# Kernel optimization log

Hardware: AMD Instinct MI355X
Metric: run time of the kernel (lower is better)

Reference implementation:

```python
import jax, jax.numpy as jnp
import numpy as np

B, S = 4, 2048
IN_F, OUT_F = 4096, 4096
BLK = 8
NB_IN = IN_F // BLK   # 512
NB_OUT = OUT_F // BLK  # 512


def setup_inputs() -> dict:
    key = jax.random.key(0)
    k_x, k_c = jax.random.split(key)
    x = jax.random.normal(k_x, (B, S, IN_F), dtype=jnp.float32)
    # mimic xavier_uniform on (NB_OUT*NB_IN, BLK) then / sqrt(BLK)
    bound = float(np.sqrt(6.0 / (NB_OUT * NB_IN + BLK)))
    circ_params = jax.random.uniform(k_c, (NB_OUT, NB_IN, BLK), dtype=jnp.float32,
                                     minval=-bound, maxval=bound) / np.sqrt(BLK)
    bias = jnp.zeros((OUT_F,), dtype=jnp.float32)
    return {"x": x, "circ_params": circ_params, "bias": bias}


def reference(x, circ_params, bias):
    # x: (B, S, IN_F) -> (B, S, NB_IN, BLK)
    xb = x.reshape(*x.shape[:-1], NB_IN, BLK)
    x_rfft = jnp.fft.rfft(xb, axis=-1)              # (B, S, NB_IN, BLK//2+1) complex
    c_rfft = jnp.fft.rfft(circ_params, axis=-1)     # (NB_OUT, NB_IN, BLK//2+1) complex
    # per-frequency block contraction: sum over input blocks i
    out_rfft = jnp.einsum('bsif,nif->bsnf', x_rfft, c_rfft)  # (B, S, NB_OUT, BLK//2+1)
    out = jnp.fft.irfft(out_rfft, n=BLK, axis=-1)   # (B, S, NB_OUT, BLK)
    out = out.reshape(*x.shape[:-1], OUT_F)
    return out + bias
```

## Files before the change

kernel.cpp:

```cpp
#include <hip/hip_runtime.h>

#define AS1 __attribute__((address_space(1)))
#define AS3 __attribute__((address_space(3)))

typedef __attribute__((ext_vector_type(8))) short short8;
typedef __attribute__((ext_vector_type(4))) float floatx4;
typedef __attribute__((ext_vector_type(8))) unsigned short u16x8;
typedef __attribute__((ext_vector_type(4))) unsigned short u16x4;
typedef __attribute__((ext_vector_type(4))) float f32x4;

#define M_DIM 8192
#define K_DIM 4096
#define N_DIM 4096
#define NB    512

#define SQ2H 0.70710678118654752f

#define P0_OFF 0
#define P1_OFF 4194304
#define P2_OFF 12582912
#define P3_OFF 20971520
#define P4_OFF 29360128
#define Q0_OFF 0
#define Q1_OFF 262144
#define Q2_OFF 1310720
#define Q3_OFF 2359296
#define Q4_OFF 3407872

static __device__ __forceinline__ unsigned short f32_to_bf16(float f) {
  union { float f; unsigned int u; } v;
  v.f = f;
  return (unsigned short)((v.u + 0x7FFFu + ((v.u >> 16) & 1u)) >> 16);
}
static __device__ __forceinline__ float bf16_to_f32(unsigned short h) {
  union { unsigned int u; float f; } v;
  v.u = ((unsigned int)h) << 16;
  return v.f;
}

struct F8 { float a0, a4, r1, i1, r2, i2, r3, i3; };
static __device__ __forceinline__ F8 rfft8(const float* x) {
  F8 o;
  o.a0 = x[0]+x[1]+x[2]+x[3]+x[4]+x[5]+x[6]+x[7];
  o.a4 = x[0]-x[1]+x[2]-x[3]+x[4]-x[5]+x[6]-x[7];
  const float d1 = x[1]-x[3]-x[5]+x[7];
  const float s1 = x[1]+x[3]-x[5]-x[7];
  o.r1 = x[0]-x[4] + SQ2H*d1;
  o.i1 = -(SQ2H*s1 + x[2]-x[6]);
  o.r2 = x[0]-x[2]+x[4]-x[6];
  o.i2 = -(x[1]-x[3]+x[5]-x[7]);
  o.r3 = x[0]-x[4] - SQ2H*d1;
  o.i3 = -(SQ2H*s1 - x[2]+x[6]);
  return o;
}


__global__ __launch_bounds__(256) void xtransform_kernel(
    const float* __restrict__ x, unsigned short* __restrict__ XF)
{
  const int tid = blockIdx.x * 256 + threadIdx.x;
  const int m  = tid >> 7;
  const int i4 = tid & 127;
  float v[32];
#pragma unroll
  for (int q = 0; q < 8; ++q)
    *reinterpret_cast<f32x4*>(v + q * 4) =
        *reinterpret_cast<const f32x4*>(x + (size_t)m * 4096 + i4 * 32 + q * 4);

  u16x4 p0, p4;
  u16x8 p1, p2, p3;
#pragma unroll
  for (int g = 0; g < 4; ++g) {
    F8 f = rfft8(v + g * 8);
    p0[g] = f32_to_bf16(f.a0);
    p4[g] = f32_to_bf16(f.a4);
    p1[2*g] = f32_to_bf16(f.r1); p1[2*g+1] = f32_to_bf16(f.i1);
    p2[2*g] = f32_to_bf16(f.r2); p2[2*g+1] = f32_to_bf16(f.i2);
    p3[2*g] = f32_to_bf16(f.r3); p3[2*g+1] = f32_to_bf16(f.i3);
  }
  *reinterpret_cast<u16x4*>(XF + P0_OFF + (size_t)m * 512 + i4 * 4) = p0;
  *reinterpret_cast<u16x4*>(XF + P4_OFF + (size_t)m * 512 + i4 * 4) = p4;
  *reinterpret_cast<u16x8*>(XF + P1_OFF + (size_t)m * 1024 + i4 * 8) = p1;
  *reinterpret_cast<u16x8*>(XF + P2_OFF + (size_t)m * 1024 + i4 * 8) = p2;
  *reinterpret_cast<u16x8*>(XF + P3_OFF + (size_t)m * 1024 + i4 * 8) = p3;
}

__global__ __launch_bounds__(256) void wtransform_kernel(
    const float* __restrict__ c, unsigned short* __restrict__ WF)
{
  const int tid = blockIdx.x * 256 + threadIdx.x;
  const int n = tid >> 9;
  const int i = tid & 511;
  float v[8];
  *reinterpret_cast<f32x4*>(v)     = *reinterpret_cast<const f32x4*>(c + (size_t)tid * 8);
  *reinterpret_cast<f32x4*>(v + 4) = *reinterpret_cast<const f32x4*>(c + (size_t)tid * 8 + 4);
  F8 f = rfft8(v);
  WF[Q0_OFF + (size_t)n * 512 + i] = f32_to_bf16(f.a0);
  WF[Q4_OFF + (size_t)n * 512 + i] = f32_to_bf16(f.a4);
  unsigned int q1or = (unsigned int)f32_to_bf16(f.r1) | ((unsigned int)f32_to_bf16(-f.i1) << 16);
  unsigned int q1oi = (unsigned int)f32_to_bf16(f.i1) | ((unsigned int)f32_to_bf16(f.r1) << 16);
  unsigned int q2or = (unsigned int)f32_to_bf16(f.r2) | ((unsigned int)f32_to_bf16(-f.i2) << 16);
  unsigned int q2oi = (unsigned int)f32_to_bf16(f.i2) | ((unsigned int)f32_to_bf16(f.r2) << 16);
  unsigned int q3or = (unsigned int)f32_to_bf16(f.r3) | ((unsigned int)f32_to_bf16(-f.i3) << 16);
  unsigned int q3oi = (unsigned int)f32_to_bf16(f.i3) | ((unsigned int)f32_to_bf16(f.r3) << 16);
  *reinterpret_cast<unsigned int*>(WF + Q1_OFF + (size_t)n * 1024 + 2 * i)         = q1or;
  *reinterpret_cast<unsigned int*>(WF + Q1_OFF + (size_t)(512 + n) * 1024 + 2 * i) = q1oi;
  *reinterpret_cast<unsigned int*>(WF + Q2_OFF + (size_t)n * 1024 + 2 * i)         = q2or;
  *reinterpret_cast<unsigned int*>(WF + Q2_OFF + (size_t)(512 + n) * 1024 + 2 * i) = q2oi;
  *reinterpret_cast<unsigned int*>(WF + Q3_OFF + (size_t)n * 1024 + 2 * i)         = q3or;
  *reinterpret_cast<unsigned int*>(WF + Q3_OFF + (size_t)(512 + n) * 1024 + 2 * i) = q3oi;
}

__global__ __launch_bounds__(256) void gemm_freq_kernel(
    const unsigned short* __restrict__ XF,
    const unsigned short* __restrict__ WF,
    unsigned short* __restrict__ OF)
{
  const int bid = blockIdx.x;
  const int swz = (bid & 7) * 256 + (bid >> 3);
  const int mt  = swz >> 5;
  const int yf  = swz & 31;
  int z, nt;
  if (yf < 4)       { z = 0; nt = yf; }
  else if (yf < 28) { z = 1 + ((yf - 4) >> 3); nt = (yf - 4) & 7; }
  else              { z = 4; nt = yf - 28; }

  int K, aoff, boff;
  switch (z) {
    case 0:  K = 512;  aoff = P0_OFF; boff = Q0_OFF; break;
    case 1:  K = 1024; aoff = P1_OFF; boff = Q1_OFF; break;
    case 2:  K = 1024; aoff = P2_OFF; boff = Q2_OFF; break;
    case 3:  K = 1024; aoff = P3_OFF; boff = Q3_OFF; break;
    default: K = 512;  aoff = P4_OFF; boff = Q4_OFF; break;
  }
  const int n0 = nt * 128;
  const int m0 = mt * 128;

  const unsigned short* A  = XF + aoff;
  const unsigned short* Bm = WF + boff;
  unsigned short* C        = OF + aoff;

  __shared__ alignas(16) unsigned short As[128 * 32];
  __shared__ alignas(16) unsigned short Bs[128 * 32];

  const int tid  = threadIdx.x;
  const int lane = tid & 63;
  const int wave = tid >> 6;
  const int wm   = wave >> 1;
  const int wn   = wave & 1;
  const int quad = lane >> 4;
  const int l15  = lane & 15;

  floatx4 acc[4][4];
#pragma unroll
  for (int i = 0; i < 4; ++i)
#pragma unroll
    for (int j = 0; j < 4; ++j) acc[i][j] = (floatx4){0.f, 0.f, 0.f, 0.f};

  for (int k0 = 0; k0 < K; k0 += 32) {
#pragma unroll
    for (int j = 0; j < 2; ++j) {
      const int chunk = j * 256 + wave * 64 + lane;
      const int row   = chunk >> 2;
      const int kc    = (chunk & 3) << 3;
      const unsigned short* ga = A  + (size_t)(m0 + row) * K + (k0 + kc);
      const unsigned short* gb = Bm + (size_t)(n0 + row) * K + (k0 + kc);
      unsigned short* la = As + (j * 256 + wave * 64) * 8;
      unsigned short* lb = Bs + (j * 256 + wave * 64) * 8;
      __builtin_amdgcn_global_load_lds((AS1 void*)ga, (AS3 void*)la, 16, 0, 0);
      __builtin_amdgcn_global_load_lds((AS1 void*)gb, (AS3 void*)lb, 16, 0, 0);
    }
    __syncthreads();

    short8 af[4], bf[4];
#pragma unroll
    for (int mi = 0; mi < 4; ++mi)
      af[mi] = *reinterpret_cast<const short8*>(As + (wm * 64 + mi * 16 + l15) * 32 + quad * 8);
#pragma unroll
    for (int ni = 0; ni < 4; ++ni)
      bf[ni] = *reinterpret_cast<const short8*>(Bs + (wn * 64 + ni * 16 + l15) * 32 + quad * 8);

#pragma unroll
    for (int mi = 0; mi < 4; ++mi)
#pragma unroll
      for (int ni = 0; ni < 4; ++ni)
        acc[mi][ni] = __builtin_amdgcn_mfma_f32_16x16x32_bf16(
            af[mi], bf[ni], acc[mi][ni], 0, 0, 0);
    __syncthreads();
  }

#pragma unroll
  for (int mi = 0; mi < 4; ++mi) {
#pragma unroll
    for (int r = 0; r < 4; ++r) {
      const int grow = m0 + wm * 64 + mi * 16 + quad * 4 + r;
      unsigned short* crow = C + (size_t)grow * K;
#pragma unroll
      for (int ni = 0; ni < 4; ++ni)
        crow[n0 + wn * 64 + ni * 16 + l15] = f32_to_bf16(acc[mi][ni][r]);
    }
  }
}

__global__ __launch_bounds__(256) void irfft_kernel(
    const unsigned short* __restrict__ OF,
    const float* __restrict__ bias,
    float* __restrict__ out)
{
  __shared__ alignas(16) float lds[256 * 36];
  const int t   = threadIdx.x;
  const int gt  = blockIdx.x * 256 + t;
  const int m   = gt >> 7;
  const int nb4 = gt & 127;

  const u16x4 a0v = *reinterpret_cast<const u16x4*>(OF + P0_OFF + (size_t)m * 512 + nb4 * 4);
  const u16x4 a4v = *reinterpret_cast<const u16x4*>(OF + P4_OFF + (size_t)m * 512 + nb4 * 4);
  const u16x4 r1v = *reinterpret_cast<const u16x4*>(OF + P1_OFF + (size_t)m * 1024 + nb4 * 4);
  const u16x4 i1v = *reinterpret_cast<const u16x4*>(OF + P1_OFF + (size_t)m * 1024 + 512 + nb4 * 4);
  const u16x4 r2v = *reinterpret_cast<const u16x4*>(OF + P2_OFF + (size_t)m * 1024 + nb4 * 4);
  const u16x4 i2v = *reinterpret_cast<const u16x4*>(OF + P2_OFF + (size_t)m * 1024 + 512 + nb4 * 4);
  const u16x4 r3v = *reinterpret_cast<const u16x4*>(OF + P3_OFF + (size_t)m * 1024 + nb4 * 4);
  const u16x4 i3v = *reinterpret_cast<const u16x4*>(OF + P3_OFF + (size_t)m * 1024 + 512 + nb4 * 4);

  float res[32];
#pragma unroll
  for (int j = 0; j < 4; ++j) {
    const int nblk = nb4 * 4 + j;
    const float a0 = bf16_to_f32(a0v[j]), a4 = bf16_to_f32(a4v[j]);
    const float r1 = bf16_to_f32(r1v[j]), i1 = bf16_to_f32(i1v[j]);
    const float r2 = bf16_to_f32(r2v[j]), i2 = bf16_to_f32(i2v[j]);
    const float r3 = bf16_to_f32(r3v[j]), i3 = bf16_to_f32(i3v[j]);

    const float ep = a0 + a4, em = a0 - a4;
    const float sr1 = SQ2H * r1, si1 = SQ2H * i1;
    const float sr3 = SQ2H * r3, si3 = SQ2H * i3;
    float o[8];
    o[0] = (ep + 2.f * ( r1 + r2 + r3)) * 0.125f;
    o[1] = (em + 2.f * ( sr1 - si1 - i2 - sr3 - si3)) * 0.125f;
    o[2] = (ep + 2.f * (-i1 - r2 + i3)) * 0.125f;
    o[3] = (em + 2.f * (-sr1 - si1 + i2 + sr3 - si3)) * 0.125f;
    o[4] = (ep + 2.f * (-r1 + r2 - r3)) * 0.125f;
    o[5] = (em + 2.f * (-sr1 + si1 - i2 + sr3 + si3)) * 0.125f;
    o[6] = (ep + 2.f * ( i1 - r2 - i3)) * 0.125f;
    o[7] = (em + 2.f * ( sr1 + si1 + i2 - sr3 + si3)) * 0.125f;

    const f32x4 blo = *reinterpret_cast<const f32x4*>(bias + nblk * 8);
    const f32x4 bhi = *reinterpret_cast<const f32x4*>(bias + nblk * 8 + 4);
#pragma unroll
    for (int k = 0; k < 4; ++k) {
      res[j * 8 + k]     = o[k]     + blo[k];
      res[j * 8 + 4 + k] = o[k + 4] + bhi[k];
    }
  }

  float* dst = lds + t * 36;
#pragma unroll
  for (int p = 0; p < 8; ++p)
    *reinterpret_cast<f32x4*>(dst + p * 4) = *reinterpret_cast<const f32x4*>(res + p * 4);
  __syncthreads();

  float* gbase = out + (size_t)blockIdx.x * 8192;
#pragma unroll
  for (int s = 0; s < 8; ++s) {
    const int off16 = s * 256 + t;
    const f32x4 vv = *reinterpret_cast<const f32x4*>(
        lds + (off16 >> 3) * 36 + (off16 & 7) * 4);
    *reinterpret_cast<f32x4*>(gbase + off16 * 4) = vv;
  }
}


__global__ __launch_bounds__(256) void convert_x_kernel(
    const float* __restrict__ x, unsigned short* __restrict__ Xb)
{
  const size_t t = (size_t)blockIdx.x * 256 + threadIdx.x;
  const f32x4 a = *reinterpret_cast<const f32x4*>(x + t * 8);
  const f32x4 b = *reinterpret_cast<const f32x4*>(x + t * 8 + 4);
  union { u16x8 v; unsigned short s[8]; } o;
#pragma unroll
  for (int u = 0; u < 4; ++u) { o.s[u] = f32_to_bf16(a[u]); o.s[u + 4] = f32_to_bf16(b[u]); }
  *reinterpret_cast<u16x8*>(Xb + t * 8) = o.v;
}

__global__ __launch_bounds__(256) void expand_w_kernel(
    const float* __restrict__ c, unsigned short* __restrict__ W)
{
  const int tid = blockIdx.x * 256 + threadIdx.x;
  const int o = tid >> 9, i = tid & 511, n = o >> 3, t = o & 7;
  const float* src = c + ((size_t)(n * NB + i) << 3);
  float raw[8];
  *reinterpret_cast<f32x4*>(raw)     = *reinterpret_cast<const f32x4*>(src);
  *reinterpret_cast<f32x4*>(raw + 4) = *reinterpret_cast<const f32x4*>(src + 4);
  union { u16x8 v; unsigned short s[8]; } outv;
#pragma unroll
  for (int u = 0; u < 8; ++u) outv.s[u] = f32_to_bf16(raw[(t - u) & 7]);
  *reinterpret_cast<u16x8*>(W + (size_t)o * K_DIM + i * 8) = outv.v;
}

__global__ __launch_bounds__(256) void gemm_bt_kernel(
    const unsigned short* __restrict__ A, const unsigned short* __restrict__ Bm,
    const float* __restrict__ bias, float* __restrict__ C)
{
  __shared__ alignas(16) unsigned short As[128 * 32];
  __shared__ alignas(16) unsigned short Bs[128 * 32];
  const int tid = threadIdx.x, lane = tid & 63, wave = tid >> 6;
  const int wm = wave >> 1, wn = wave & 1;
  const int m0 = blockIdx.y * 128, n0 = blockIdx.x * 128;
  const int quad = lane >> 4, l15 = lane & 15;

  floatx4 acc[4][4];
#pragma unroll
  for (int i = 0; i < 4; ++i)
#pragma unroll
    for (int j = 0; j < 4; ++j) acc[i][j] = (floatx4){0.f, 0.f, 0.f, 0.f};

  for (int k0 = 0; k0 < K_DIM; k0 += 32) {
#pragma unroll
    for (int j = 0; j < 2; ++j) {
      const int chunk = j * 256 + wave * 64 + lane;
      const int row = chunk >> 2, kc = (chunk & 3) << 3;
      const unsigned short* ga = A  + (size_t)(m0 + row) * K_DIM + (k0 + kc);
      const unsigned short* gb = Bm + (size_t)(n0 + row) * K_DIM + (k0 + kc);
      unsigned short* la = As + (j * 256 + wave * 64) * 8;
      unsigned short* lb = Bs + (j * 256 + wave * 64) * 8;
      __builtin_amdgcn_global_load_lds((AS1 void*)ga, (AS3 void*)la, 16, 0, 0);
      __builtin_amdgcn_global_load_lds((AS1 void*)gb, (AS3 void*)lb, 16, 0, 0);
    }
    __syncthreads();
    short8 af[4], bf[4];
#pragma unroll
    for (int mi = 0; mi < 4; ++mi)
      af[mi] = *reinterpret_cast<const short8*>(As + (wm * 64 + mi * 16 + l15) * 32 + quad * 8);
#pragma unroll
    for (int ni = 0; ni < 4; ++ni)
      bf[ni] = *reinterpret_cast<const short8*>(Bs + (wn * 64 + ni * 16 + l15) * 32 + quad * 8);
#pragma unroll
    for (int mi = 0; mi < 4; ++mi)
#pragma unroll
      for (int ni = 0; ni < 4; ++ni)
        acc[mi][ni] = __builtin_amdgcn_mfma_f32_16x16x32_bf16(af[mi], bf[ni], acc[mi][ni], 0, 0, 0);
    __syncthreads();
  }
  float bv[4]; int cols[4];
#pragma unroll
  for (int ni = 0; ni < 4; ++ni) { cols[ni] = n0 + wn * 64 + ni * 16 + l15; bv[ni] = bias[cols[ni]]; }
#pragma unroll
  for (int mi = 0; mi < 4; ++mi)
#pragma unroll
    for (int r = 0; r < 4; ++r) {
      const int grow = m0 + wm * 64 + mi * 16 + quad * 4 + r;
      float* crow = C + (size_t)grow * N_DIM;
#pragma unroll
      for (int ni = 0; ni < 4; ++ni) crow[cols[ni]] = acc[mi][ni][r] + bv[ni];
    }
}

extern "C" void kernel_launch(void* const* d_in, const int* in_sizes, int n_in,
                              void* d_out, int out_size, void* d_ws, size_t ws_size,
                              hipStream_t stream) {
  const float* x    = (const float*)d_in[0];
  const float* circ = (const float*)d_in[1];
  const float* bias = (const float*)d_in[2];
  float* out = (float*)d_out;

  const size_t XF_BYTES = (size_t)33554432 * 2;
  const size_t WF_BYTES = (size_t)3670016 * 2;
  const size_t OF_BYTES = (size_t)33554432 * 2;
  const size_t NEED = XF_BYTES + WF_BYTES + OF_BYTES;

  if (ws_size >= NEED) {
    unsigned short* XF = (unsigned short*)d_ws;
    unsigned short* WF = (unsigned short*)((char*)d_ws + XF_BYTES);
    unsigned short* OF = (unsigned short*)((char*)d_ws + XF_BYTES + WF_BYTES);

    wtransform_kernel<<<(NB * NB) / 256, 256, 0, stream>>>(circ, WF);
    xtransform_kernel<<<(M_DIM * NB / 4) / 256, 256, 0, stream>>>(x, XF);
    gemm_freq_kernel<<<2048, 256, 0, stream>>>(XF, WF, OF);
    irfft_kernel<<<M_DIM / 2, 256, 0, stream>>>(OF, bias, out);
  } else {
    unsigned short* W  = (unsigned short*)d_ws;
    unsigned short* Xb = (unsigned short*)((char*)d_ws + (size_t)N_DIM * K_DIM * 2);
    convert_x_kernel<<<(M_DIM * K_DIM / 8) / 256, 256, 0, stream>>>(x, Xb);
    expand_w_kernel<<<(N_DIM * NB) / 256, 256, 0, stream>>>(circ, W);
    dim3 grid(N_DIM / 128, M_DIM / 128);
    gemm_bt_kernel<<<grid, 256, 0, stream>>>(Xb, W, bias, out);
  }
}
```

Measured before the change: 363.6 us.

## Coalesce x loads through swizzled LDS and double GEMM K-tile with XOR swizzle

```diff
diff --git a/kernel.cpp b/kernel.cpp
--- a/kernel.cpp
+++ b/kernel.cpp
@@ -58,15 +58,31 @@
 __global__ __launch_bounds__(256) void xtransform_kernel(
     const float* __restrict__ x, unsigned short* __restrict__ XF)
 {
-  const int tid = blockIdx.x * 256 + threadIdx.x;
-  const int m  = tid >> 7;
-  const int i4 = tid & 127;
+  __shared__ alignas(16) float lds[8192];
+  const int t  = threadIdx.x;
+  const int m0 = blockIdx.x * 2;
+  const float* src = x + (size_t)m0 * 4096;
+
+#pragma unroll
+  for (int s = 0; s < 8; ++s) {
+    const int u  = s * 256 + t;
+    const int pu = u ^ ((u >> 3) & 7);
+    *reinterpret_cast<f32x4*>(lds + pu * 4) =
+        *reinterpret_cast<const f32x4*>(src + (size_t)u * 4);
+  }
+  __syncthreads();
+
+  const int r  = t >> 7;
+  const int i4 = t & 127;
   float v[32];
 #pragma unroll
-  for (int q = 0; q < 8; ++q)
-    *reinterpret_cast<f32x4*>(v + q * 4) =
-        *reinterpret_cast<const f32x4*>(x + (size_t)m * 4096 + i4 * 32 + q * 4);
-
+  for (int p = 0; p < 8; ++p) {
+    const int u  = r * 1024 + i4 * 8 + p;
+    const int pu = u ^ ((u >> 3) & 7);
+    *reinterpret_cast<f32x4*>(v + p * 4) = *reinterpret_cast<const f32x4*>(lds + pu * 4);
+  }
+
+  const int m = m0 + r;
   u16x4 p0, p4;
   u16x8 p1, p2, p3;
 #pragma unroll
@@ -140,8 +156,8 @@
   const unsigned short* Bm = WF + boff;
   unsigned short* C        = OF + aoff;
 
-  __shared__ alignas(16) unsigned short As[128 * 32];
-  __shared__ alignas(16) unsigned short Bs[128 * 32];
+  __shared__ alignas(16) unsigned short As[128 * 64];
+  __shared__ alignas(16) unsigned short Bs[128 * 64];
 
   const int tid  = threadIdx.x;
   const int lane = tid & 63;
@@ -150,6 +166,7 @@
   const int wn   = wave & 1;
   const int quad = lane >> 4;
   const int l15  = lane & 15;
+  const int par4 = (l15 & 1) << 2;
 
   floatx4 acc[4][4];
 #pragma unroll
@@ -157,35 +174,36 @@
 #pragma unroll
     for (int j = 0; j < 4; ++j) acc[i][j] = (floatx4){0.f, 0.f, 0.f, 0.f};
 
-  for (int k0 = 0; k0 < K; k0 += 32) {
-#pragma unroll
-    for (int j = 0; j < 2; ++j) {
-      const int chunk = j * 256 + wave * 64 + lane;
-      const int row   = chunk >> 2;
-      const int kc    = (chunk & 3) << 3;
-      const unsigned short* ga = A  + (size_t)(m0 + row) * K + (k0 + kc);
-      const unsigned short* gb = Bm + (size_t)(n0 + row) * K + (k0 + kc);
-      unsigned short* la = As + (j * 256 + wave * 64) * 8;
-      unsigned short* lb = Bs + (j * 256 + wave * 64) * 8;
-      __builtin_amdgcn_global_load_lds((AS1 void*)ga, (AS3 void*)la, 16, 0, 0);
-      __builtin_amdgcn_global_load_lds((AS1 void*)gb, (AS3 void*)lb, 16, 0, 0);
+  for (int k0 = 0; k0 < K; k0 += 64) {
+#pragma unroll
+    for (int j = 0; j < 4; ++j) {
+      const int c   = j * 256 + wave * 64 + lane;
+      const int row = c >> 3;
+      const int lu  = (c & 7) ^ ((row & 1) << 2);
+      const unsigned short* ga = A  + (size_t)(m0 + row) * K + k0 + lu * 8;
+      const unsigned short* gb = Bm + (size_t)(n0 + row) * K + k0 + lu * 8;
+      __builtin_amdgcn_global_load_lds((AS1 void*)ga, (AS3 void*)(As + c * 8), 16, 0, 0);
+      __builtin_amdgcn_global_load_lds((AS1 void*)gb, (AS3 void*)(Bs + c * 8), 16, 0, 0);
     }
     __syncthreads();
 
-    short8 af[4], bf[4];
-#pragma unroll
-    for (int mi = 0; mi < 4; ++mi)
-      af[mi] = *reinterpret_cast<const short8*>(As + (wm * 64 + mi * 16 + l15) * 32 + quad * 8);
-#pragma unroll
-    for (int ni = 0; ni < 4; ++ni)
-      bf[ni] = *reinterpret_cast<const short8*>(Bs + (wn * 64 + ni * 16 + l15) * 32 + quad * 8);
-
-#pragma unroll
-    for (int mi = 0; mi < 4; ++mi)
+#pragma unroll
+    for (int s = 0; s < 2; ++s) {
+      const int u = (s * 4 + quad) ^ par4;
+      short8 af[4], bf[4];
+#pragma unroll
+      for (int mi = 0; mi < 4; ++mi)
+        af[mi] = *reinterpret_cast<const short8*>(As + (wm * 64 + mi * 16 + l15) * 64 + u * 8);
 #pragma unroll
       for (int ni = 0; ni < 4; ++ni)
-        acc[mi][ni] = __builtin_amdgcn_mfma_f32_16x16x32_bf16(
-            af[mi], bf[ni], acc[mi][ni], 0, 0, 0);
+        bf[ni] = *reinterpret_cast<const short8*>(Bs + (wn * 64 + ni * 16 + l15) * 64 + u * 8);
+#pragma unroll
+      for (int mi = 0; mi < 4; ++mi)
+#pragma unroll
+        for (int ni = 0; ni < 4; ++ni)
+          acc[mi][ni] = __builtin_amdgcn_mfma_f32_16x16x32_bf16(
+              af[mi], bf[ni], acc[mi][ni], 0, 0, 0);
+    }
     __syncthreads();
   }
 
@@ -374,7 +392,7 @@
     unsigned short* OF = (unsigned short*)((char*)d_ws + XF_BYTES + WF_BYTES);
 
     wtransform_kernel<<<(NB * NB) / 256, 256, 0, stream>>>(circ, WF);
-    xtransform_kernel<<<(M_DIM * NB / 4) / 256, 256, 0, stream>>>(x, XF);
+    xtransform_kernel<<<M_DIM / 2, 256, 0, stream>>>(x, XF);
     gemm_freq_kernel<<<2048, 256, 0, stream>>>(XF, WF, OF);
     irfft_kernel<<<M_DIM / 2, 256, 0, stream>>>(OF, bias, out);
   } else {
```

Result: faster. 348.4 us (-4.2%).
